# Performance work log

Measured on AMD Instinct MI355X. Metric: run time of the kernel, lower is better.

Reference implementation:

```python
import jax, jax.numpy as jnp
import numpy as np

B, LQ, LK, D = 4, 256, 256, 768


def setup_inputs() -> dict:
    key = jax.random.key(0)
    ks = jax.random.split(key, 11)
    s = 1.0 / np.sqrt(D)
    return {
        "query": jax.random.normal(ks[0], (B, LQ, D), jnp.float32),
        "key": jax.random.normal(ks[1], (B, LK, D), jnp.float32),
        "value": jax.random.normal(ks[2], (B, LK, D), jnp.float32),
        "Wq": jax.random.uniform(ks[3], (D, D), jnp.float32, -s, s),
        "bq": jax.random.uniform(ks[4], (D,), jnp.float32, -s, s),
        "Wk": jax.random.uniform(ks[5], (D, D), jnp.float32, -s, s),
        "bk": jax.random.uniform(ks[6], (D,), jnp.float32, -s, s),
        "Wv": jax.random.uniform(ks[7], (D, D), jnp.float32, -s, s),
        "bv": jax.random.uniform(ks[8], (D,), jnp.float32, -s, s),
        "Ws": jax.random.uniform(ks[9], (D,), jnp.float32, -s, s),
        "bs": jax.random.uniform(ks[10], (), jnp.float32, -s, s),
    }


def reference(query, key, value, Wq, bq, Wk, bk, Wv, bv, Ws, bs):
    # Linear projections (torch Linear: x @ W.T + b; here W stored as [in, out])
    q = jnp.einsum('bqd,de->bqe', query, Wq) + bq   # [B,Lq,D]
    k = jnp.einsum('bkd,de->bke', key, Wk) + bk     # [B,Lk,D]
    v = jnp.einsum('bkd,de->bke', value, Wv) + bv   # [B,Lk,D]
    # Additive (Bahdanau) scores: tanh(q_i + k_j) . Ws + bs  -> [B,Lq,Lk]
    h = jnp.tanh(q[:, :, None, :] + k[:, None, :, :])  # [B,Lq,Lk,D]
    scores = jnp.einsum('bqkd,d->bqk', h, Ws) + bs
    attention_weights = jax.nn.softmax(scores, axis=-1)  # [B,Lq,Lk]
    attended = jnp.einsum('bqk,bkd->bqd', attention_weights, v)
    return attended, attention_weights
```

## Files before the change

### kernel.cpp

```cpp
#include <hip/hip_runtime.h>

#define NB 4
#define SLQ 256
#define SLK 256
#define DD 768

#define TWO_LOG2E 2.8853900817779268f
#define LOG2E 1.4426950408889634f

typedef _Float16 f16x4 __attribute__((ext_vector_type(4)));
typedef _Float16 f16x8 __attribute__((ext_vector_type(8)));
typedef float f32x4 __attribute__((ext_vector_type(4)));

__device__ __forceinline__ float fexp2(float x) { return __builtin_amdgcn_exp2f(x); }
__device__ __forceinline__ float frcp(float x) { return __builtin_amdgcn_rcpf(x); }

#define LSTR 40
#define TSTR 72
#define TFSTR 65
#define NPS  ((size_t)NB * SLQ * SLK)

__global__ __launch_bounds__(256) void prep_wt_kernel(
    const float* __restrict__ Wq, const float* __restrict__ Wk,
    const float* __restrict__ Wv, _Float16* __restrict__ wtq,
    _Float16* __restrict__ wtk, _Float16* __restrict__ wtv)
{
    const int z = blockIdx.z;
    const float* W = (z == 0) ? Wq : (z == 1) ? Wk : Wv;
    _Float16* Wt = (z == 0) ? wtq : (z == 1) ? wtk : wtv;

    __shared__ float t[64][65];
    const int tid = threadIdx.x;
    const int kt0 = blockIdx.y * 64;
    const int nt0 = blockIdx.x * 64;

    const int col4 = (tid & 15) << 2;
#pragma unroll
    for (int i = 0; i < 4; ++i) {
        const int row = ((tid >> 4) << 2) + i;
        *(float4*)&t[row][col4] = *(const float4*)&W[(size_t)(kt0 + row) * DD + nt0 + col4];
    }
    __syncthreads();
    const int n = tid >> 2;
    const int k16 = (tid & 3) << 4;
    f16x8 h0, h1;
#pragma unroll
    for (int j = 0; j < 8; ++j) {
        h0[j] = (_Float16)t[k16 + j][n];
        h1[j] = (_Float16)t[k16 + 8 + j][n];
    }
    *(f16x8*)&Wt[(size_t)(nt0 + n) * DD + kt0 + k16] = h0;
    *(f16x8*)&Wt[(size_t)(nt0 + n) * DD + kt0 + k16 + 8] = h1;
}

__global__ __launch_bounds__(256) void qkv_f16_kernel(
    const float* __restrict__ query, const float* __restrict__ key_in,
    const float* __restrict__ value, const _Float16* __restrict__ wtq,
    const _Float16* __restrict__ wtk, const _Float16* __restrict__ wtv,
    const float* __restrict__ bq, const float* __restrict__ bk,
    const float* __restrict__ bv, float* __restrict__ eq,
    _Float16* __restrict__ ekc, _Float16* __restrict__ vsht)
{
    const int z = blockIdx.z;
    const float* A = (z == 0) ? query : (z == 1) ? key_in : value;
    const _Float16* Wt = (z == 0) ? wtq : (z == 1) ? wtk : wtv;
    const float* bias = (z == 0) ? bq : (z == 1) ? bk : bv;

    __shared__ _Float16 Sh[2][2][64 * LSTR];

    const int tid = threadIdx.x;
    const int lane = tid & 63;
    const int wid = tid >> 6;
    const int wr = wid >> 1;
    const int wc = wid & 1;
    const int row0 = blockIdx.y * 64;
    const int col0 = blockIdx.x * 64;

    const int sr = tid >> 2;
    const int sc = (tid & 3) << 3;

    const float* Ap = A + (size_t)(row0 + sr) * DD + sc;
    const _Float16* Bp = Wt + (size_t)(col0 + sr) * DD + sc;

    float4 pa0 = *(const float4*)Ap;
    float4 pa1 = *(const float4*)(Ap + 4);
    f16x8 pb = *(const f16x8*)Bp;

    f32x4 acc[2][2] = {};
    const int kj = (lane >> 4) << 3;
    const int fr = lane & 15;

    {
        f16x8 ha;
        ha[0] = (_Float16)pa0.x; ha[1] = (_Float16)pa0.y;
        ha[2] = (_Float16)pa0.z; ha[3] = (_Float16)pa0.w;
        ha[4] = (_Float16)pa1.x; ha[5] = (_Float16)pa1.y;
        ha[6] = (_Float16)pa1.z; ha[7] = (_Float16)pa1.w;
        *(f16x8*)&Sh[0][0][sr * LSTR + sc] = ha;
        *(f16x8*)&Sh[0][1][sr * LSTR + sc] = pb;
    }
    __syncthreads();

    int p = 0;
    for (int s = 0; s < DD / 32; ++s) {
        if (s + 1 < DD / 32) {
            pa0 = *(const float4*)(Ap + (s + 1) * 32);
            pa1 = *(const float4*)(Ap + (s + 1) * 32 + 4);
            pb = *(const f16x8*)(Bp + (s + 1) * 32);
        }
        f16x8 af0 = *(const f16x8*)&Sh[p][0][(wr * 32 + fr) * LSTR + kj];
        f16x8 af1 = *(const f16x8*)&Sh[p][0][(wr * 32 + 16 + fr) * LSTR + kj];
        f16x8 bf0 = *(const f16x8*)&Sh[p][1][(wc * 32 + fr) * LSTR + kj];
        f16x8 bf1 = *(const f16x8*)&Sh[p][1][(wc * 32 + 16 + fr) * LSTR + kj];
        acc[0][0] = __builtin_amdgcn_mfma_f32_16x16x32_f16(af0, bf0, acc[0][0], 0, 0, 0);
        acc[0][1] = __builtin_amdgcn_mfma_f32_16x16x32_f16(af0, bf1, acc[0][1], 0, 0, 0);
        acc[1][0] = __builtin_amdgcn_mfma_f32_16x16x32_f16(af1, bf0, acc[1][0], 0, 0, 0);
        acc[1][1] = __builtin_amdgcn_mfma_f32_16x16x32_f16(af1, bf1, acc[1][1], 0, 0, 0);
        if (s + 1 < DD / 32) {
            f16x8 ha;
            ha[0] = (_Float16)pa0.x; ha[1] = (_Float16)pa0.y;
            ha[2] = (_Float16)pa0.z; ha[3] = (_Float16)pa0.w;
            ha[4] = (_Float16)pa1.x; ha[5] = (_Float16)pa1.y;
            ha[6] = (_Float16)pa1.z; ha[7] = (_Float16)pa1.w;
            *(f16x8*)&Sh[p ^ 1][0][sr * LSTR + sc] = ha;
            *(f16x8*)&Sh[p ^ 1][1][sr * LSTR + sc] = pb;
        }
        __syncthreads();
        p ^= 1;
    }

    const int clb = wc * 32 + fr;
    const int rlb = wr * 32 + ((lane >> 4) << 2);

    if (z < 2) {
        float* Tf = (float*)Sh;
#pragma unroll
        for (int mf = 0; mf < 2; ++mf) {
#pragma unroll
            for (int nf = 0; nf < 2; ++nf) {
                const int cl = clb + nf * 16;
                const float bvv = bias[col0 + cl];
#pragma unroll
                for (int r = 0; r < 4; ++r) {
                    const int rl = rlb + mf * 16 + r;
                    const float arg = fminf((acc[mf][nf][r] + bvv) * TWO_LOG2E, 15.0f);
                    Tf[rl * TFSTR + cl] = fexp2(arg);
                }
            }
        }
        __syncthreads();
        if (z == 0) {
#pragma unroll
            for (int j = 0; j < 4; ++j) {
                const int u = tid + j * 256;
                const int row = u >> 4;
                const int c4 = (u & 15) << 2;
                float4 v = *(const float4*)&Tf[row * TFSTR + c4];
                *(float4*)&eq[(size_t)(row0 + row) * DD + col0 + c4] = v;
            }
        } else {
            const int b = row0 >> 8;
            const int krow0 = row0 & 255;
            const size_t base = (size_t)b * (SLK * DD) + (size_t)(col0 >> 3) * (SLK * 8);
#pragma unroll
            for (int j = 0; j < 2; ++j) {
                const int u = tid + j * 256;
                const int c2 = u >> 6;
                const int k = u & 63;
                const float* src = &Tf[k * TFSTR + c2 * 8];
                f16x8 h;
#pragma unroll
                for (int i = 0; i < 8; ++i) h[i] = (_Float16)src[i];
                *(f16x8*)&ekc[base + (size_t)c2 * (SLK * 8) + (size_t)(krow0 + k) * 8] = h;
            }
        }
    } else {
        _Float16* T = (_Float16*)Sh;
#pragma unroll
        for (int mf = 0; mf < 2; ++mf) {
#pragma unroll
            for (int nf = 0; nf < 2; ++nf) {
                const int cl = clb + nf * 16;
                const float bvv = bias[col0 + cl];
                const int rl = rlb + mf * 16;
                f16x4 h;
#pragma unroll
                for (int r = 0; r < 4; ++r) h[r] = (_Float16)(acc[mf][nf][r] + bvv);
                *(f16x4*)&T[cl * TSTR + rl] = h;
            }
        }
        __syncthreads();
        const int b = row0 >> 8;
        const int krow0 = row0 & 255;
#pragma unroll
        for (int j = 0; j < 2; ++j) {
            const int u = tid + 256 * j;
            const int c2 = u >> 3;
            const int g = u & 7;
            f16x8 hv = *(const f16x8*)&T[c2 * TSTR + g * 8];
            *(f16x8*)&vsht[((size_t)b * DD + col0 + c2) * SLK + krow0 + g * 8] = hv;
        }
    }
}

__global__ __launch_bounds__(256) void scores_partial_kernel(
    const float* __restrict__ Eq, const _Float16* __restrict__ Ekc,
    const float* __restrict__ Ws, float* __restrict__ pbuf)
{
    const int bz = blockIdx.z;
    const int b = bz >> 2;
    const int s = bz & 3;
    const int k0 = blockIdx.x * 64;
    const int q0 = blockIdx.y * 8;
    const int lane = threadIdx.x & 63;
    const int wid = __builtin_amdgcn_readfirstlane((int)(threadIdx.x >> 6));
    const int q = q0 + (wid << 1);
    const int d0 = s * 192;

    const _Float16* kr = Ekc + (size_t)b * (SLK * DD) + ((d0 >> 3) * (SLK * 8)) +
                         (k0 + lane) * 8;
    const float* qp0 = Eq + (size_t)(b * SLQ + q) * DD + d0;
    const float* qp1 = qp0 + DD;
    const float* wp = Ws + d0;

    float acc0 = 0.f, acc1 = 0.f;

#pragma unroll 4
    for (int c = 0; c < 24; ++c) {
        const int dn = c * 8;
        f16x8 e = *(const f16x8*)(kr + (size_t)c * (SLK * 8));
        float4 ga0 = *(const float4*)(qp0 + dn);
        float4 ga1 = *(const float4*)(qp0 + dn + 4);
        float4 gb0 = *(const float4*)(qp1 + dn);
        float4 gb1 = *(const float4*)(qp1 + dn + 4);
        float4 w0 = *(const float4*)(wp + dn);
        float4 w1 = *(const float4*)(wp + dn + 4);

        float e0 = (float)e[0], e1 = (float)e[1], e2 = (float)e[2], e3 = (float)e[3];
        float e4 = (float)e[4], e5 = (float)e[5], e6 = (float)e[6], e7 = (float)e[7];

        {
            float A0 = fmaf(ga0.x, e0, 1.0f), A1 = fmaf(ga0.y, e1, 1.0f);
            float A2 = fmaf(ga0.z, e2, 1.0f), A3 = fmaf(ga0.w, e3, 1.0f);
            float A4 = fmaf(ga1.x, e4, 1.0f), A5 = fmaf(ga1.y, e5, 1.0f);
            float A6 = fmaf(ga1.z, e6, 1.0f), A7 = fmaf(ga1.w, e7, 1.0f);
            acc0 = fmaf(fmaf(w0.x, A1, w0.y * A0), frcp(A0 * A1), acc0);
            acc0 = fmaf(fmaf(w0.z, A3, w0.w * A2), frcp(A2 * A3), acc0);
            acc0 = fmaf(fmaf(w1.x, A5, w1.y * A4), frcp(A4 * A5), acc0);
            acc0 = fmaf(fmaf(w1.z, A7, w1.w * A6), frcp(A6 * A7), acc0);
        }
        {
            float A0 = fmaf(gb0.x, e0, 1.0f), A1 = fmaf(gb0.y, e1, 1.0f);
            float A2 = fmaf(gb0.z, e2, 1.0f), A3 = fmaf(gb0.w, e3, 1.0f);
            float A4 = fmaf(gb1.x, e4, 1.0f), A5 = fmaf(gb1.y, e5, 1.0f);
            float A6 = fmaf(gb1.z, e6, 1.0f), A7 = fmaf(gb1.w, e7, 1.0f);
            acc1 = fmaf(fmaf(w0.x, A1, w0.y * A0), frcp(A0 * A1), acc1);
            acc1 = fmaf(fmaf(w0.z, A3, w0.w * A2), frcp(A2 * A3), acc1);
            acc1 = fmaf(fmaf(w1.x, A5, w1.y * A4), frcp(A4 * A5), acc1);
            acc1 = fmaf(fmaf(w1.z, A7, w1.w * A6), frcp(A6 * A7), acc1);
        }
    }

    const size_t o = (size_t)s * NPS + (size_t)(b * SLQ + q) * SLK + k0 + lane;
    pbuf[o] = -2.0f * acc0;
    pbuf[o + SLK] = -2.0f * acc1;
}

__global__ __launch_bounds__(256) void softmax_combine_kernel(
    const float* __restrict__ pbuf, float* __restrict__ attnw,
    _Float16* __restrict__ phalf)
{
    const int lane = threadIdx.x & 63;
    const int wv = threadIdx.x >> 6;
    const int row = blockIdx.x * 4 + wv;
    const size_t base = (size_t)row * SLK + (lane << 2);

    float4 x0 = *(const float4*)&pbuf[base];
    float4 x1 = *(const float4*)&pbuf[base + NPS];
    float4 x2 = *(const float4*)&pbuf[base + 2 * NPS];
    float4 x3 = *(const float4*)&pbuf[base + 3 * NPS];
    float4 x;
    x.x = (x0.x + x1.x) + (x2.x + x3.x);
    x.y = (x0.y + x1.y) + (x2.y + x3.y);
    x.z = (x0.z + x1.z) + (x2.z + x3.z);
    x.w = (x0.w + x1.w) + (x2.w + x3.w);

    float m = fmaxf(fmaxf(x.x, x.y), fmaxf(x.z, x.w));
#pragma unroll
    for (int off = 32; off; off >>= 1) m = fmaxf(m, __shfl_xor(m, off, 64));

    float e0 = fexp2((x.x - m) * LOG2E);
    float e1 = fexp2((x.y - m) * LOG2E);
    float e2 = fexp2((x.z - m) * LOG2E);
    float e3 = fexp2((x.w - m) * LOG2E);
    float sm = (e0 + e1) + (e2 + e3);
#pragma unroll
    for (int off = 32; off; off >>= 1) sm += __shfl_xor(sm, off, 64);

    const float inv = 1.0f / sm;
    float4 o;
    o.x = e0 * inv; o.y = e1 * inv; o.z = e2 * inv; o.w = e3 * inv;
    *(float4*)&attnw[base] = o;

    f16x4 h;
    h[0] = (_Float16)o.x; h[1] = (_Float16)o.y;
    h[2] = (_Float16)o.z; h[3] = (_Float16)o.w;
    *(f16x4*)&phalf[base] = h;
}

__global__ __launch_bounds__(256) void attended_f16_kernel(
    const _Float16* __restrict__ phalf, const _Float16* __restrict__ vsht,
    float* __restrict__ out)
{
    const int row0 = blockIdx.y * 64;
    const int col0 = blockIdx.x * 32;
    const int b = row0 >> 8;
    const _Float16* Bt = vsht + (size_t)b * DD * SLK;
    float* C = out + (size_t)(row0)*DD;

    __shared__ _Float16 Ah[2][64 * LSTR];
    __shared__ _Float16 Bh[2][32 * LSTR];

    const int tid = threadIdx.x;
    const int lane = tid & 63;
    const int wid = tid >> 6;

    const int sr = tid >> 2;
    const int sc = (tid & 3) << 3;
    const int br = tid >> 2;
    const int bc = (tid & 3) << 3;

    const _Float16* Ap = phalf + (size_t)(row0 + sr) * SLK + sc;
    const _Float16* Bp = Bt + (size_t)(col0 + br) * SLK + bc;

    f16x8 pa = *(const f16x8*)Ap;
    f16x8 pb;
    if (tid < 128) pb = *(const f16x8*)Bp;

    f32x4 acc0 = {}, acc1 = {};
    const int kj = (lane >> 4) << 3;
    const int fr = lane & 15;

    *(f16x8*)&Ah[0][sr * LSTR + sc] = pa;
    if (tid < 128) *(f16x8*)&Bh[0][br * LSTR + bc] = pb;
    __syncthreads();

    int p = 0;
    for (int s = 0; s < SLK / 32; ++s) {
        if (s + 1 < SLK / 32) {
            pa = *(const f16x8*)(Ap + (s + 1) * 32);
            if (tid < 128) pb = *(const f16x8*)(Bp + (s + 1) * 32);
        }
        f16x8 af = *(const f16x8*)&Ah[p][(wid * 16 + fr) * LSTR + kj];
        f16x8 bf0 = *(const f16x8*)&Bh[p][fr * LSTR + kj];
        f16x8 bf1 = *(const f16x8*)&Bh[p][(16 + fr) * LSTR + kj];
        acc0 = __builtin_amdgcn_mfma_f32_16x16x32_f16(af, bf0, acc0, 0, 0, 0);
        acc1 = __builtin_amdgcn_mfma_f32_16x16x32_f16(af, bf1, acc1, 0, 0, 0);
        if (s + 1 < SLK / 32) {
            *(f16x8*)&Ah[p ^ 1][sr * LSTR + sc] = pa;
            if (tid < 128) *(f16x8*)&Bh[p ^ 1][br * LSTR + bc] = pb;
        }
        __syncthreads();
        p ^= 1;
    }

    const int colb = col0 + fr;
    const int rowb = wid * 16 + ((lane >> 4) << 2);
#pragma unroll
    for (int r = 0; r < 4; ++r) {
        C[(size_t)(rowb + r) * DD + colb] = acc0[r];
        C[(size_t)(rowb + r) * DD + colb + 16] = acc1[r];
    }
}

extern "C" void kernel_launch(void* const* d_in, const int* in_sizes, int n_in,
                              void* d_out, int out_size, void* d_ws, size_t ws_size,
                              hipStream_t stream)
{
    (void)in_sizes; (void)n_in; (void)out_size; (void)ws_size;

    const float* query = (const float*)d_in[0];
    const float* key   = (const float*)d_in[1];
    const float* value = (const float*)d_in[2];
    const float* Wq = (const float*)d_in[3];
    const float* bq = (const float*)d_in[4];
    const float* Wk = (const float*)d_in[5];
    const float* bk = (const float*)d_in[6];
    const float* Wv = (const float*)d_in[7];
    const float* bv = (const float*)d_in[8];
    const float* Ws = (const float*)d_in[9];

    const size_t NE = (size_t)NB * SLQ * DD;
    const size_t NW = (size_t)DD * DD;

    char* w = (char*)d_ws;
    float* eq = (float*)w;               w += NE * 4;
    _Float16* ekc = (_Float16*)w;        w += NE * 2;
    _Float16* vsht = (_Float16*)w;       w += NE * 2;
    _Float16* phalf = (_Float16*)w;      w += NPS * 2;
    _Float16* wtq = (_Float16*)w;        w += NW * 2;
    _Float16* wtk = (_Float16*)w;        w += NW * 2;
    _Float16* wtv = (_Float16*)w;        w += NW * 2;
    float* pbuf = (float*)w;

    float* out = (float*)d_out;
    float* attended = out;
    float* attnw = out + NE;

    prep_wt_kernel<<<dim3(DD / 64, DD / 64, 3), 256, 0, stream>>>(
        Wq, Wk, Wv, wtq, wtk, wtv);
    qkv_f16_kernel<<<dim3(DD / 64, (NB * SLQ) / 64, 3), 256, 0, stream>>>(
        query, key, value, wtq, wtk, wtv, bq, bk, bv, eq, ekc, vsht);
    scores_partial_kernel<<<dim3(SLK / 64, SLQ / 8, NB * 4), 256, 0, stream>>>(
        eq, ekc, Ws, pbuf);
    softmax_combine_kernel<<<dim3((NB * SLQ) / 4), 256, 0, stream>>>(
        pbuf, attnw, phalf);
    attended_f16_kernel<<<dim3(DD / 32, (NB * SLQ) / 64, 1), 256, 0, stream>>>(
        phalf, vsht, attended);
}
```

Baseline: 133.4 us.

## Fuse softmax into attended GEMM and deepen QKV GEMM K-step to 64

The softmax-combine kernel is merged into the attention-times-V kernel. Each block reduces the four partial score buffers for its 64 rows, computes the softmax in registers, and stages the f16 probabilities and a 32-column V slice in shared memory before running the MFMA loop with no further syncs. This removes one launch and the phalf round trip through global memory. In exchange, every one of the 24 column blocks recomputes softmax over the same rows and rereads pbuf, so pbuf traffic grows by roughly 24x, much of it likely served from L2. Separately, the QKV GEMM stages 64-wide K tiles instead of 32, halving the loop iterations and barriers at the cost of more shared memory.

Measured after the change: 149.3 us. 11.9% more time.

```diff
diff --git a/kernel.cpp b/kernel.cpp
--- a/kernel.cpp
+++ b/kernel.cpp
@@ -15,9 +15,10 @@
 __device__ __forceinline__ float fexp2(float x) { return __builtin_amdgcn_exp2f(x); }
 __device__ __forceinline__ float frcp(float x) { return __builtin_amdgcn_rcpf(x); }
 
-#define LSTR 40
+#define KSTR 72
 #define TSTR 72
 #define TFSTR 65
+#define PSTR 264
 #define NPS  ((size_t)NB * SLQ * SLK)
 
 __global__ __launch_bounds__(256) void prep_wt_kernel(
@@ -66,7 +67,7 @@
     const _Float16* Wt = (z == 0) ? wtq : (z == 1) ? wtk : wtv;
     const float* bias = (z == 0) ? bq : (z == 1) ? bk : bv;
 
-    __shared__ _Float16 Sh[2][2][64 * LSTR];
+    __shared__ _Float16 Sh[2][2][64 * KSTR];
 
     const int tid = threadIdx.x;
     const int lane = tid & 63;
@@ -77,14 +78,17 @@
     const int col0 = blockIdx.x * 64;
 
     const int sr = tid >> 2;
-    const int sc = (tid & 3) << 3;
+    const int sc = (tid & 3) << 4;
 
     const float* Ap = A + (size_t)(row0 + sr) * DD + sc;
     const _Float16* Bp = Wt + (size_t)(col0 + sr) * DD + sc;
 
     float4 pa0 = *(const float4*)Ap;
     float4 pa1 = *(const float4*)(Ap + 4);
-    f16x8 pb = *(const f16x8*)Bp;
+    float4 pa2 = *(const float4*)(Ap + 8);
+    float4 pa3 = *(const float4*)(Ap + 12);
+    f16x8 pb0 = *(const f16x8*)Bp;
+    f16x8 pb1 = *(const f16x8*)(Bp + 8);
 
     f32x4 acc[2][2] = {};
     const int kj = (lane >> 4) << 3;
@@ -96,34 +100,54 @@
         ha[2] = (_Float16)pa0.z; ha[3] = (_Float16)pa0.w;
         ha[4] = (_Float16)pa1.x; ha[5] = (_Float16)pa1.y;
         ha[6] = (_Float16)pa1.z; ha[7] = (_Float16)pa1.w;
-        *(f16x8*)&Sh[0][0][sr * LSTR + sc] = ha;
-        *(f16x8*)&Sh[0][1][sr * LSTR + sc] = pb;
+        *(f16x8*)&Sh[0][0][sr * KSTR + sc] = ha;
+        ha[0] = (_Float16)pa2.x; ha[1] = (_Float16)pa2.y;
+        ha[2] = (_Float16)pa2.z; ha[3] = (_Float16)pa2.w;
+        ha[4] = (_Float16)pa3.x; ha[5] = (_Float16)pa3.y;
+        ha[6] = (_Float16)pa3.z; ha[7] = (_Float16)pa3.w;
+        *(f16x8*)&Sh[0][0][sr * KSTR + sc + 8] = ha;
+        *(f16x8*)&Sh[0][1][sr * KSTR + sc] = pb0;
+        *(f16x8*)&Sh[0][1][sr * KSTR + sc + 8] = pb1;
     }
     __syncthreads();
 
     int p = 0;
-    for (int s = 0; s < DD / 32; ++s) {
-        if (s + 1 < DD / 32) {
-            pa0 = *(const float4*)(Ap + (s + 1) * 32);
-            pa1 = *(const float4*)(Ap + (s + 1) * 32 + 4);
-            pb = *(const f16x8*)(Bp + (s + 1) * 32);
-        }
-        f16x8 af0 = *(const f16x8*)&Sh[p][0][(wr * 32 + fr) * LSTR + kj];
-        f16x8 af1 = *(const f16x8*)&Sh[p][0][(wr * 32 + 16 + fr) * LSTR + kj];
-        f16x8 bf0 = *(const f16x8*)&Sh[p][1][(wc * 32 + fr) * LSTR + kj];
-        f16x8 bf1 = *(const f16x8*)&Sh[p][1][(wc * 32 + 16 + fr) * LSTR + kj];
-        acc[0][0] = __builtin_amdgcn_mfma_f32_16x16x32_f16(af0, bf0, acc[0][0], 0, 0, 0);
-        acc[0][1] = __builtin_amdgcn_mfma_f32_16x16x32_f16(af0, bf1, acc[0][1], 0, 0, 0);
-        acc[1][0] = __builtin_amdgcn_mfma_f32_16x16x32_f16(af1, bf0, acc[1][0], 0, 0, 0);
-        acc[1][1] = __builtin_amdgcn_mfma_f32_16x16x32_f16(af1, bf1, acc[1][1], 0, 0, 0);
-        if (s + 1 < DD / 32) {
+    for (int s = 0; s < DD / 64; ++s) {
+        if (s + 1 < DD / 64) {
+            const int ks = (s + 1) * 64;
+            pa0 = *(const float4*)(Ap + ks);
+            pa1 = *(const float4*)(Ap + ks + 4);
+            pa2 = *(const float4*)(Ap + ks + 8);
+            pa3 = *(const float4*)(Ap + ks + 12);
+            pb0 = *(const f16x8*)(Bp + ks);
+            pb1 = *(const f16x8*)(Bp + ks + 8);
+        }
+#pragma unroll
+        for (int h = 0; h < 2; ++h) {
+            const int ko = h * 32 + kj;
+            f16x8 af0 = *(const f16x8*)&Sh[p][0][(wr * 32 + fr) * KSTR + ko];
+            f16x8 af1 = *(const f16x8*)&Sh[p][0][(wr * 32 + 16 + fr) * KSTR + ko];
+            f16x8 bf0 = *(const f16x8*)&Sh[p][1][(wc * 32 + fr) * KSTR + ko];
+            f16x8 bf1 = *(const f16x8*)&Sh[p][1][(wc * 32 + 16 + fr) * KSTR + ko];
+            acc[0][0] = __builtin_amdgcn_mfma_f32_16x16x32_f16(af0, bf0, acc[0][0], 0, 0, 0);
+            acc[0][1] = __builtin_amdgcn_mfma_f32_16x16x32_f16(af0, bf1, acc[0][1], 0, 0, 0);
+            acc[1][0] = __builtin_amdgcn_mfma_f32_16x16x32_f16(af1, bf0, acc[1][0], 0, 0, 0);
+            acc[1][1] = __builtin_amdgcn_mfma_f32_16x16x32_f16(af1, bf1, acc[1][1], 0, 0, 0);
+        }
+        if (s + 1 < DD / 64) {
             f16x8 ha;
             ha[0] = (_Float16)pa0.x; ha[1] = (_Float16)pa0.y;
             ha[2] = (_Float16)pa0.z; ha[3] = (_Float16)pa0.w;
             ha[4] = (_Float16)pa1.x; ha[5] = (_Float16)pa1.y;
             ha[6] = (_Float16)pa1.z; ha[7] = (_Float16)pa1.w;
-            *(f16x8*)&Sh[p ^ 1][0][sr * LSTR + sc] = ha;
-            *(f16x8*)&Sh[p ^ 1][1][sr * LSTR + sc] = pb;
+            *(f16x8*)&Sh[p ^ 1][0][sr * KSTR + sc] = ha;
+            ha[0] = (_Float16)pa2.x; ha[1] = (_Float16)pa2.y;
+            ha[2] = (_Float16)pa2.z; ha[3] = (_Float16)pa2.w;
+            ha[4] = (_Float16)pa3.x; ha[5] = (_Float16)pa3.y;
+            ha[6] = (_Float16)pa3.z; ha[7] = (_Float16)pa3.w;
+            *(f16x8*)&Sh[p ^ 1][0][sr * KSTR + sc + 8] = ha;
+            *(f16x8*)&Sh[p ^ 1][1][sr * KSTR + sc] = pb0;
+            *(f16x8*)&Sh[p ^ 1][1][sr * KSTR + sc + 8] = pb1;
         }
         __syncthreads();
         p ^= 1;
@@ -266,106 +290,107 @@
     pbuf[o + SLK] = -2.0f * acc1;
 }
 
-__global__ __launch_bounds__(256) void softmax_combine_kernel(
-    const float* __restrict__ pbuf, float* __restrict__ attnw,
-    _Float16* __restrict__ phalf)
+__global__ __launch_bounds__(256) void attended_fused_kernel(
+    const float* __restrict__ pbuf, const _Float16* __restrict__ vsht,
+    float* __restrict__ attnw, float* __restrict__ out)
 {
-    const int lane = threadIdx.x & 63;
-    const int wv = threadIdx.x >> 6;
-    const int row = blockIdx.x * 4 + wv;
-    const size_t base = (size_t)row * SLK + (lane << 2);
-
-    float4 x0 = *(const float4*)&pbuf[base];
-    float4 x1 = *(const float4*)&pbuf[base + NPS];
-    float4 x2 = *(const float4*)&pbuf[base + 2 * NPS];
-    float4 x3 = *(const float4*)&pbuf[base + 3 * NPS];
-    float4 x;
-    x.x = (x0.x + x1.x) + (x2.x + x3.x);
-    x.y = (x0.y + x1.y) + (x2.y + x3.y);
-    x.z = (x0.z + x1.z) + (x2.z + x3.z);
-    x.w = (x0.w + x1.w) + (x2.w + x3.w);
-
-    float m = fmaxf(fmaxf(x.x, x.y), fmaxf(x.z, x.w));
-#pragma unroll
-    for (int off = 32; off; off >>= 1) m = fmaxf(m, __shfl_xor(m, off, 64));
-
-    float e0 = fexp2((x.x - m) * LOG2E);
-    float e1 = fexp2((x.y - m) * LOG2E);
-    float e2 = fexp2((x.z - m) * LOG2E);
-    float e3 = fexp2((x.w - m) * LOG2E);
-    float sm = (e0 + e1) + (e2 + e3);
-#pragma unroll
-    for (int off = 32; off; off >>= 1) sm += __shfl_xor(sm, off, 64);
-
-    const float inv = 1.0f / sm;
-    float4 o;
-    o.x = e0 * inv; o.y = e1 * inv; o.z = e2 * inv; o.w = e3 * inv;
-    *(float4*)&attnw[base] = o;
-
-    f16x4 h;
-    h[0] = (_Float16)o.x; h[1] = (_Float16)o.y;
-    h[2] = (_Float16)o.z; h[3] = (_Float16)o.w;
-    *(f16x4*)&phalf[base] = h;
-}
-
-__global__ __launch_bounds__(256) void attended_f16_kernel(
-    const _Float16* __restrict__ phalf, const _Float16* __restrict__ vsht,
-    float* __restrict__ out)
-{
+    __shared__ _Float16 Pl[64 * PSTR];
+    __shared__ _Float16 Vl[32 * PSTR];
+
+    const int tid = threadIdx.x;
     const int row0 = blockIdx.y * 64;
     const int col0 = blockIdx.x * 32;
     const int b = row0 >> 8;
-    const _Float16* Bt = vsht + (size_t)b * DD * SLK;
-    float* C = out + (size_t)(row0)*DD;
-
-    __shared__ _Float16 Ah[2][64 * LSTR];
-    __shared__ _Float16 Bh[2][32 * LSTR];
-
-    const int tid = threadIdx.x;
+
+    const int rid = tid >> 2;
+    const int part = tid & 3;
+    const size_t base = (size_t)(row0 + rid) * SLK + part * 64;
+
+    float4 v[16];
+#pragma unroll
+    for (int j = 0; j < 16; ++j) {
+        float4 a = *(const float4*)&pbuf[base + j * 4];
+        float4 c1 = *(const float4*)&pbuf[base + j * 4 + NPS];
+        float4 c2 = *(const float4*)&pbuf[base + j * 4 + 2 * NPS];
+        float4 c3 = *(const float4*)&pbuf[base + j * 4 + 3 * NPS];
+        v[j].x = (a.x + c1.x) + (c2.x + c3.x);
+        v[j].y = (a.y + c1.y) + (c2.y + c3.y);
+        v[j].z = (a.z + c1.z) + (c2.z + c3.z);
+        v[j].w = (a.w + c1.w) + (c2.w + c3.w);
+    }
+    float m = -3.0e38f;
+#pragma unroll
+    for (int j = 0; j < 16; ++j)
+        m = fmaxf(m, fmaxf(fmaxf(v[j].x, v[j].y), fmaxf(v[j].z, v[j].w)));
+    m = fmaxf(m, __shfl_xor(m, 1, 64));
+    m = fmaxf(m, __shfl_xor(m, 2, 64));
+
+    float s = 0.f;
+#pragma unroll
+    for (int j = 0; j < 16; ++j) {
+        v[j].x = fexp2((v[j].x - m) * LOG2E);
+        v[j].y = fexp2((v[j].y - m) * LOG2E);
+        v[j].z = fexp2((v[j].z - m) * LOG2E);
+        v[j].w = fexp2((v[j].w - m) * LOG2E);
+        s += (v[j].x + v[j].y) + (v[j].z + v[j].w);
+    }
+    s += __shfl_xor(s, 1, 64);
+    s += __shfl_xor(s, 2, 64);
+    const float inv = 1.0f / s;
+
+    const bool write_attn = (blockIdx.x == 0);
+#pragma unroll
+    for (int j = 0; j < 16; j += 2) {
+        float4 p0, p1;
+        p0.x = v[j].x * inv; p0.y = v[j].y * inv;
+        p0.z = v[j].z * inv; p0.w = v[j].w * inv;
+        p1.x = v[j + 1].x * inv; p1.y = v[j + 1].y * inv;
+        p1.z = v[j + 1].z * inv; p1.w = v[j + 1].w * inv;
+        f16x8 h;
+        h[0] = (_Float16)p0.x; h[1] = (_Float16)p0.y;
+        h[2] = (_Float16)p0.z; h[3] = (_Float16)p0.w;
+        h[4] = (_Float16)p1.x; h[5] = (_Float16)p1.y;
+        h[6] = (_Float16)p1.z; h[7] = (_Float16)p1.w;
+        *(f16x8*)&Pl[rid * PSTR + part * 64 + j * 4] = h;
+        if (write_attn) {
+            *(float4*)&attnw[base + j * 4] = p0;
+            *(float4*)&attnw[base + j * 4 + 4] = p1;
+        }
+    }
+
+    {
+        const _Float16* Bt = vsht + ((size_t)b * DD + col0) * SLK;
+#pragma unroll
+        for (int i = 0; i < 4; ++i) {
+            const int u = tid + i * 256;
+            const int c = u >> 5;
+            const int kseg = (u & 31) << 3;
+            *(f16x8*)&Vl[c * PSTR + kseg] = *(const f16x8*)&Bt[(size_t)c * SLK + kseg];
+        }
+    }
+
+    __syncthreads();
+
     const int lane = tid & 63;
     const int wid = tid >> 6;
-
-    const int sr = tid >> 2;
-    const int sc = (tid & 3) << 3;
-    const int br = tid >> 2;
-    const int bc = (tid & 3) << 3;
-
-    const _Float16* Ap = phalf + (size_t)(row0 + sr) * SLK + sc;
-    const _Float16* Bp = Bt + (size_t)(col0 + br) * SLK + bc;
-
-    f16x8 pa = *(const f16x8*)Ap;
-    f16x8 pb;
-    if (tid < 128) pb = *(const f16x8*)Bp;
+    const int fr = lane & 15;
+    const int kj = (lane >> 4) << 3;
+    const int band = wid << 4;
 
     f32x4 acc0 = {}, acc1 = {};
-    const int kj = (lane >> 4) << 3;
-    const int fr = lane & 15;
-
-    *(f16x8*)&Ah[0][sr * LSTR + sc] = pa;
-    if (tid < 128) *(f16x8*)&Bh[0][br * LSTR + bc] = pb;
-    __syncthreads();
-
-    int p = 0;
-    for (int s = 0; s < SLK / 32; ++s) {
-        if (s + 1 < SLK / 32) {
-            pa = *(const f16x8*)(Ap + (s + 1) * 32);
-            if (tid < 128) pb = *(const f16x8*)(Bp + (s + 1) * 32);
-        }
-        f16x8 af = *(const f16x8*)&Ah[p][(wid * 16 + fr) * LSTR + kj];
-        f16x8 bf0 = *(const f16x8*)&Bh[p][fr * LSTR + kj];
-        f16x8 bf1 = *(const f16x8*)&Bh[p][(16 + fr) * LSTR + kj];
+#pragma unroll
+    for (int ks = 0; ks < 8; ++ks) {
+        const int ko = ks * 32 + kj;
+        f16x8 af = *(const f16x8*)&Pl[(band + fr) * PSTR + ko];
+        f16x8 bf0 = *(const f16x8*)&Vl[fr * PSTR + ko];
+        f16x8 bf1 = *(const f16x8*)&Vl[(16 + fr) * PSTR + ko];
         acc0 = __builtin_amdgcn_mfma_f32_16x16x32_f16(af, bf0, acc0, 0, 0, 0);
         acc1 = __builtin_amdgcn_mfma_f32_16x16x32_f16(af, bf1, acc1, 0, 0, 0);
-        if (s + 1 < SLK / 32) {
-            *(f16x8*)&Ah[p ^ 1][sr * LSTR + sc] = pa;
-            if (tid < 128) *(f16x8*)&Bh[p ^ 1][br * LSTR + bc] = pb;
-        }
-        __syncthreads();
-        p ^= 1;
-    }
-
+    }
+
+    float* C = out + (size_t)row0 * DD;
     const int colb = col0 + fr;
-    const int rowb = wid * 16 + ((lane >> 4) << 2);
+    const int rowb = band + ((lane >> 4) << 2);
 #pragma unroll
     for (int r = 0; r < 4; ++r) {
         C[(size_t)(rowb + r) * DD + colb] = acc0[r];
@@ -397,7 +422,6 @@
     float* eq = (float*)w;               w += NE * 4;
     _Float16* ekc = (_Float16*)w;        w += NE * 2;
     _Float16* vsht = (_Float16*)w;       w += NE * 2;
-    _Float16* phalf = (_Float16*)w;      w += NPS * 2;
     _Float16* wtq = (_Float16*)w;        w += NW * 2;
     _Float16* wtk = (_Float16*)w;        w += NW * 2;
     _Float16* wtv = (_Float16*)w;        w += NW * 2;
@@ -413,8 +437,6 @@
         query, key, value, wtq, wtk, wtv, bq, bk, bv, eq, ekc, vsht);
     scores_partial_kernel<<<dim3(SLK / 64, SLQ / 8, NB * 4), 256, 0, stream>>>(
         eq, ekc, Ws, pbuf);
-    softmax_combine_kernel<<<dim3((NB * SLQ) / 4), 256, 0, stream>>>(
-        pbuf, attnw, phalf);
-    attended_f16_kernel<<<dim3(DD / 32, (NB * SLQ) / 64, 1), 256, 0, stream>>>(
-        phalf, vsht, attended);
+    attended_fused_kernel<<<dim3(DD / 32, (NB * SLQ) / 64, 1), 256, 0, stream>>>(
+        pbuf, vsht, attnw, attended);
 }
```
